# Kernel optimization log

Hardware: AMD Instinct MI355X
Metric: run time of the kernel (lower is better)

## Reference

```python
import jax, jax.numpy as jnp
import numpy as np

N_CELLS = 500_000
B = 512
D_X = 128
D_Z = 32
D_IN = D_X + D_Z  # 160
H = 256
D_OUT = 16


def _linear_params(key, fan_in, fan_out):
    k1, k2 = jax.random.split(key)
    bound = 1.0 / np.sqrt(fan_in)
    W = jax.random.uniform(k1, (fan_in, fan_out), jnp.float32, -bound, bound)
    b = jax.random.uniform(k2, (fan_out,), jnp.float32, -bound, bound)
    return W, b


def setup_inputs() -> dict:
    key = jax.random.key(0)
    ks = jax.random.split(key, 8)
    X = jax.random.uniform(ks[0], (N_CELLS, D_X), jnp.float32)  # nonneg counts-like
    Z = jax.random.normal(ks[1], (B, D_Z), jnp.float32)
    cell_to_batch = jax.random.randint(ks[2], (N_CELLS,), 0, B, jnp.int64)
    sample_idx_batch = jnp.arange(B, dtype=jnp.int64)
    W1, b1 = _linear_params(ks[3], D_IN, H)
    W2, b2 = _linear_params(ks[4], H, H)
    W3, b3 = _linear_params(ks[5], H, D_OUT)
    return {"X": X, "Z": Z, "W1": W1, "b1": b1, "W2": W2, "b2": b2,
            "W3": W3, "b3": b3, "cell_to_batch": cell_to_batch,
            "sample_idx_batch": sample_idx_batch}


def reference(X, Z, W1, b1, W2, b2, W3, b3, cell_to_batch, sample_idx_batch):
    # gather per-sample covariates to per-cell rows
    Zc = Z[cell_to_batch]                              # [N, D_Z]
    seg = sample_idx_batch[cell_to_batch]              # [N] remapped sample ids
    # preprocessor: log-normalize X, concat covariates
    Xp = jnp.concatenate([jnp.log1p(X), Zc], axis=-1)  # [N, D_IN]
    # cell predictor MLP (Linear-ReLU x2 + Linear)
    h = jax.nn.relu(Xp @ W1 + b1)
    h = jax.nn.relu(h @ W2 + b2)
    X_cell = h @ W3 + b3                               # [N, D_OUT]
    # aggregator: segment mean over cells of each sample
    nseg = sample_idx_batch.shape[0]
    sums = jax.ops.segment_sum(X_cell, seg, num_segments=nseg)
    counts = jax.ops.segment_sum(jnp.ones((X_cell.shape[0], 1), X_cell.dtype), seg, num_segments=nseg)
    Y_sample = sums / jnp.maximum(counts, 1.0)
    # postprocessor: identity
    return Y_sample
```

## Files before the change

### kernel.cpp

```cpp
#include <hip/hip_runtime.h>
#include <hip/hip_bf16.h>

typedef __attribute__((ext_vector_type(8))) short short8;
typedef __attribute__((ext_vector_type(4))) short short4v;
typedef __attribute__((ext_vector_type(4))) float floatx4;

#define N_CELLS  500000
#define B_SAMP   512
#define D_X      128
#define D_Z      32
#define H_DIM    256
#define D_OUT    16

#define M_TILE   64
#define NBLK     7813
#define LDA      136
#define LDH      264
#define SP_LD    20

#define NREP     64

#define OFF_W1P   0
#define OFF_W2P   65536
#define OFF_W3P   196608
#define OFF_ZW    204800
#define OFF_ACC   729088
#define OFF_CNT   2826240
#define OFF_C2S   2957312

#define W1_BLKS   128
#define W2_BLKS   256
#define W3_BLKS   16
#define ZW_BLKS   512
#define C2S_BLKS  1954

__device__ __forceinline__ short bfb(float x) {
    union { __hip_bfloat16 h; short s; } u;
    u.h = __float2bfloat16(x);
    return u.s;
}

__global__ __launch_bounds__(256)
void prep(const float* __restrict__ W1, const float* __restrict__ b1,
          const float* __restrict__ W2, const float* __restrict__ W3,
          const float* __restrict__ Z,
          const int* __restrict__ c2b, const int* __restrict__ sidx,
          __hip_bfloat16* __restrict__ w1p, __hip_bfloat16* __restrict__ w2p,
          __hip_bfloat16* __restrict__ w3p, float* __restrict__ zw1,
          float* __restrict__ cnts, int* __restrict__ c2s) {
    int bid = blockIdx.x;
    int tid = threadIdx.x;
    if (bid < W1_BLKS + W2_BLKS + W3_BLKS) {
        const float* W; __hip_bfloat16* dst; int N, kS, idx; float scale;
        if (bid < W1_BLKS) {
            idx = bid * 256 + tid; W = W1; dst = w1p; N = H_DIM; kS = 4;
            scale = 0.6931471805599453f;
        } else if (bid < W1_BLKS + W2_BLKS) {
            idx = (bid - W1_BLKS) * 256 + tid; W = W2; dst = w2p; N = H_DIM; kS = 8;
            scale = 1.0f;
        } else {
            idx = (bid - W1_BLKS - W2_BLKS) * 256 + tid; W = W3; dst = w3p; N = D_OUT; kS = 8;
            scale = 1.0f;
        }
        int j = idx & 7;
        int L = (idx >> 3) & 63;
        int s = (idx >> 9) % kS;
        int t = idx / (kS << 9);
        int k = s * 32 + ((L >> 4) << 3) + j;
        int n = t * 16 + (L & 15);
        dst[idx] = __float2bfloat16(W[(size_t)k * N + n] * scale);
        return;
    }
    bid -= W1_BLKS + W2_BLKS + W3_BLKS;
    if (bid < ZW_BLKS) {
        int s = bid;
        float a = b1[tid];
        const float* zr = Z + (size_t)s * D_Z;
        const float* wr = W1 + (size_t)D_X * H_DIM + tid;
#pragma unroll 8
        for (int k = 0; k < D_Z; ++k) a += zr[k] * wr[(size_t)k * H_DIM];
        zw1[(size_t)s * H_DIM + tid] = a;
        return;
    }
    bid -= ZW_BLKS;
    int i = bid * 256 + tid;
    if (i < N_CELLS) {
        int si = sidx[c2b[i]];
        c2s[i] = si;
        atomicAdd(&cnts[(size_t)(bid & (NREP - 1)) * B_SAMP + si], 1.0f);
    }
}

__global__ __launch_bounds__(512, 6)
void fused_mlp(const float* __restrict__ X, const int* __restrict__ c2b,
               const int* __restrict__ c2s, const float* __restrict__ b2,
               const float* __restrict__ b3,
               const __hip_bfloat16* __restrict__ w1p,
               const __hip_bfloat16* __restrict__ w2p,
               const __hip_bfloat16* __restrict__ w3p,
               const float* __restrict__ zw1,
               float* __restrict__ accs, float* __restrict__ cnts) {
    __shared__ __align__(16) short sX[M_TILE * LDA];
    __shared__ short sH[M_TILE][LDH];
    __shared__ int sSI[M_TILE];
    short (*xp)[LDA] = (short (*)[LDA])sX;
    float (*sP)[M_TILE][SP_LD] = (float (*)[M_TILE][SP_LD])sX;

    const int tid = threadIdx.x;
    const int w   = tid >> 6;
    const int L   = tid & 63;
    const int q   = L >> 4;
    const int ln  = L & 15;
    const int wm  = w >> 2;
    const int wn  = w & 3;
    const int base = blockIdx.x * M_TILE;

    int g0 = base + wm * 32 + ln;      if (g0 >= N_CELLS) g0 = N_CELLS - 1;
    int g1 = base + wm * 32 + 16 + ln; if (g1 >= N_CELLS) g1 = N_CELLS - 1;
    int cb0 = c2b[g0];
    int cb1 = c2b[g1];
    floatx4 acc[2][4];
#pragma unroll
    for (int nt = 0; nt < 4; ++nt) {
        acc[0][nt] = *(const floatx4*)(zw1 + (size_t)cb0 * H_DIM + wn * 64 + nt * 16 + q * 4);
        acc[1][nt] = *(const floatx4*)(zw1 + (size_t)cb1 * H_DIM + wn * 64 + nt * 16 + q * 4);
    }

#pragma unroll
    for (int i = 0; i < 4; ++i) {
        int idx = tid + i * 512;
        int row = idx >> 5, c4 = idx & 31;
        int gr = base + row; if (gr >= N_CELLS) gr = N_CELLS - 1;
        float4 v = *(const float4*)(X + (size_t)gr * D_X + c4 * 4);
        short4v pk;
        pk.x = bfb(__log2f(1.0f + v.x));
        pk.y = bfb(__log2f(1.0f + v.y));
        pk.z = bfb(__log2f(1.0f + v.z));
        pk.w = bfb(__log2f(1.0f + v.w));
        *(short4v*)&xp[row][c4 * 4] = pk;
    }
    if ((tid & 7) == 0) {
        int row = tid >> 3;
        int gr = base + row; if (gr >= N_CELLS) gr = N_CELLS - 1;
        sSI[row] = c2s[gr];
    }
    __syncthreads();

#pragma unroll
    for (int s = 0; s < 4; ++s) {
        short8 x0 = *(const short8*)&xp[wm * 32 + ln][s * 32 + q * 8];
        short8 x1 = *(const short8*)&xp[wm * 32 + 16 + ln][s * 32 + q * 8];
#pragma unroll
        for (int nt = 0; nt < 4; ++nt) {
            short8 wf = *(const short8*)(w1p + (size_t)(((((wn * 4 + nt) * 4) + s) << 6) + L) * 8);
            acc[0][nt] = __builtin_amdgcn_mfma_f32_16x16x32_bf16(wf, x0, acc[0][nt], 0, 0, 0);
            acc[1][nt] = __builtin_amdgcn_mfma_f32_16x16x32_bf16(wf, x1, acc[1][nt], 0, 0, 0);
        }
    }
#pragma unroll
    for (int nt = 0; nt < 4; ++nt) {
        short4v p0, p1;
        p0.x = bfb(fmaxf(acc[0][nt][0], 0.f));
        p0.y = bfb(fmaxf(acc[0][nt][1], 0.f));
        p0.z = bfb(fmaxf(acc[0][nt][2], 0.f));
        p0.w = bfb(fmaxf(acc[0][nt][3], 0.f));
        p1.x = bfb(fmaxf(acc[1][nt][0], 0.f));
        p1.y = bfb(fmaxf(acc[1][nt][1], 0.f));
        p1.z = bfb(fmaxf(acc[1][nt][2], 0.f));
        p1.w = bfb(fmaxf(acc[1][nt][3], 0.f));
        *(short4v*)&sH[wm * 32 + ln][wn * 64 + nt * 16 + q * 4] = p0;
        *(short4v*)&sH[wm * 32 + 16 + ln][wn * 64 + nt * 16 + q * 4] = p1;
    }
    __syncthreads();

#pragma unroll
    for (int nt = 0; nt < 4; ++nt) {
        float4 bv = *(const float4*)(b2 + wn * 64 + nt * 16 + q * 4);
        acc[0][nt] = (floatx4){bv.x, bv.y, bv.z, bv.w};
        acc[1][nt] = acc[0][nt];
    }
#pragma unroll
    for (int s = 0; s < 8; ++s) {
        short8 x0 = *(const short8*)&sH[wm * 32 + ln][s * 32 + q * 8];
        short8 x1 = *(const short8*)&sH[wm * 32 + 16 + ln][s * 32 + q * 8];
#pragma unroll
        for (int nt = 0; nt < 4; ++nt) {
            short8 wf = *(const short8*)(w2p + (size_t)(((((wn * 4 + nt) * 8) + s) << 6) + L) * 8);
            acc[0][nt] = __builtin_amdgcn_mfma_f32_16x16x32_bf16(wf, x0, acc[0][nt], 0, 0, 0);
            acc[1][nt] = __builtin_amdgcn_mfma_f32_16x16x32_bf16(wf, x1, acc[1][nt], 0, 0, 0);
        }
    }
    __syncthreads();
#pragma unroll
    for (int nt = 0; nt < 4; ++nt) {
        short4v p0, p1;
        p0.x = bfb(fmaxf(acc[0][nt][0], 0.f));
        p0.y = bfb(fmaxf(acc[0][nt][1], 0.f));
        p0.z = bfb(fmaxf(acc[0][nt][2], 0.f));
        p0.w = bfb(fmaxf(acc[0][nt][3], 0.f));
        p1.x = bfb(fmaxf(acc[1][nt][0], 0.f));
        p1.y = bfb(fmaxf(acc[1][nt][1], 0.f));
        p1.z = bfb(fmaxf(acc[1][nt][2], 0.f));
        p1.w = bfb(fmaxf(acc[1][nt][3], 0.f));
        *(short4v*)&sH[wm * 32 + ln][wn * 64 + nt * 16 + q * 4] = p0;
        *(short4v*)&sH[wm * 32 + 16 + ln][wn * 64 + nt * 16 + q * 4] = p1;
    }
    __syncthreads();

    {
        int g  = w & 3;
        int kh = w >> 2;
        floatx4 a3 = (floatx4){0.f, 0.f, 0.f, 0.f};
#pragma unroll
        for (int ss = 0; ss < 4; ++ss) {
            int s = kh * 4 + ss;
            short8 hv = *(const short8*)&sH[g * 16 + ln][s * 32 + q * 8];
            short8 wf = *(const short8*)(w3p + (size_t)((s << 6) + L) * 8);
            a3 = __builtin_amdgcn_mfma_f32_16x16x32_bf16(wf, hv, a3, 0, 0, 0);
        }
#pragma unroll
        for (int r = 0; r < 4; ++r)
            sP[kh][g * 16 + ln][q * 4 + r] = a3[r];
    }
    __syncthreads();

    {
        int rep = blockIdx.x & (NREP - 1);
        float* accR = accs + (size_t)rep * (B_SAMP * D_OUT);
#pragma unroll
        for (int i = 0; i < 2; ++i) {
            int idx = tid + i * 512;
            int m = idx >> 4, n = idx & 15;
            int cell = base + m;
            if (cell < N_CELLS) {
                float v = sP[0][m][n] + sP[1][m][n] + b3[n];
                atomicAdd(&accR[(size_t)sSI[m] * D_OUT + n], v);
            }
        }
    }
}

__global__ __launch_bounds__(256)
void finalize(const float* __restrict__ accs, const float* __restrict__ cnts,
              float* __restrict__ out) {
    int o = blockIdx.x * blockDim.x + threadIdx.x;
    int s = o >> 4;
    float sum = 0.f, cnt = 0.f;
#pragma unroll 8
    for (int r = 0; r < NREP; ++r) {
        sum += accs[(size_t)r * (B_SAMP * D_OUT) + o];
        cnt += cnts[(size_t)r * B_SAMP + s];
    }
    out[o] = sum / fmaxf(cnt, 1.0f);
}

extern "C" void kernel_launch(void* const* d_in, const int* in_sizes, int n_in,
                              void* d_out, int out_size, void* d_ws, size_t ws_size,
                              hipStream_t stream) {
    const float* X   = (const float*)d_in[0];
    const float* Z   = (const float*)d_in[1];
    const float* W1  = (const float*)d_in[2];
    const float* b1  = (const float*)d_in[3];
    const float* W2  = (const float*)d_in[4];
    const float* b2  = (const float*)d_in[5];
    const float* W3  = (const float*)d_in[6];
    const float* b3  = (const float*)d_in[7];
    const int*   c2b = (const int*)d_in[8];
    const int*   sidx= (const int*)d_in[9];

    char* ws = (char*)d_ws;
    __hip_bfloat16* w1p = (__hip_bfloat16*)(ws + OFF_W1P);
    __hip_bfloat16* w2p = (__hip_bfloat16*)(ws + OFF_W2P);
    __hip_bfloat16* w3p = (__hip_bfloat16*)(ws + OFF_W3P);
    float* zw1  = (float*)(ws + OFF_ZW);
    float* accs = (float*)(ws + OFF_ACC);
    float* cnts = (float*)(ws + OFF_CNT);
    int*   c2s  = (int*)(ws + OFF_C2S);
    float* out  = (float*)d_out;

    hipMemsetAsync(accs, 0, (size_t)NREP * (B_SAMP * D_OUT + B_SAMP) * 4, stream);

    prep<<<W1_BLKS + W2_BLKS + W3_BLKS + ZW_BLKS + C2S_BLKS, 256, 0, stream>>>(
        W1, b1, W2, W3, Z, c2b, sidx, w1p, w2p, w3p, zw1, cnts, c2s);

    fused_mlp<<<NBLK, 512, 0, stream>>>(X, c2b, c2s, b2, b3,
                                        w1p, w2p, w3p, zw1, accs, cnts);
    finalize<<<32, 256, 0, stream>>>(accs, cnts, out);
}
```

Measured before the change: 525.7 us.

## Double cell tile to 128 rows, alias X into sH, shuffle-feed layer 3

Result: no change. 532.1 us (+1.2%).

```diff
diff --git a/kernel.cpp b/kernel.cpp
--- a/kernel.cpp
+++ b/kernel.cpp
@@ -12,9 +12,8 @@
 #define H_DIM    256
 #define D_OUT    16
 
-#define M_TILE   64
-#define NBLK     7813
-#define LDA      136
+#define M_TILE   128
+#define NBLK     3907
 #define LDH      264
 #define SP_LD    20
 
@@ -38,6 +37,9 @@
     union { __hip_bfloat16 h; short s; } u;
     u.h = __float2bfloat16(x);
     return u.s;
+}
+__device__ __forceinline__ int pack2(float a, float b) {
+    return ((int)(unsigned short)bfb(a)) | ((int)bfb(b) << 16);
 }
 
 __global__ __launch_bounds__(256)
@@ -91,7 +93,7 @@
     }
 }
 
-__global__ __launch_bounds__(512, 6)
+__global__ __launch_bounds__(512, 4)
 void fused_mlp(const float* __restrict__ X, const int* __restrict__ c2b,
                const int* __restrict__ c2s, const float* __restrict__ b2,
                const float* __restrict__ b3,
@@ -100,11 +102,9 @@
                const __hip_bfloat16* __restrict__ w3p,
                const float* __restrict__ zw1,
                float* __restrict__ accs, float* __restrict__ cnts) {
-    __shared__ __align__(16) short sX[M_TILE * LDA];
-    __shared__ short sH[M_TILE][LDH];
+    __shared__ __align__(16) short sH[M_TILE][LDH];
     __shared__ int sSI[M_TILE];
-    short (*xp)[LDA] = (short (*)[LDA])sX;
-    float (*sP)[M_TILE][SP_LD] = (float (*)[M_TILE][SP_LD])sX;
+    float (*sP)[M_TILE][SP_LD] = (float (*)[M_TILE][SP_LD])sH;
 
     const int tid = threadIdx.x;
     const int w   = tid >> 6;
@@ -115,19 +115,19 @@
     const int wn  = w & 3;
     const int base = blockIdx.x * M_TILE;
 
-    int g0 = base + wm * 32 + ln;      if (g0 >= N_CELLS) g0 = N_CELLS - 1;
-    int g1 = base + wm * 32 + 16 + ln; if (g1 >= N_CELLS) g1 = N_CELLS - 1;
-    int cb0 = c2b[g0];
-    int cb1 = c2b[g1];
-    floatx4 acc[2][4];
-#pragma unroll
-    for (int nt = 0; nt < 4; ++nt) {
-        acc[0][nt] = *(const floatx4*)(zw1 + (size_t)cb0 * H_DIM + wn * 64 + nt * 16 + q * 4);
-        acc[1][nt] = *(const floatx4*)(zw1 + (size_t)cb1 * H_DIM + wn * 64 + nt * 16 + q * 4);
-    }
-
-#pragma unroll
-    for (int i = 0; i < 4; ++i) {
+    floatx4 acc[4][4];
+#pragma unroll
+    for (int mt = 0; mt < 4; ++mt) {
+        int g = base + wm * 64 + mt * 16 + ln;
+        if (g >= N_CELLS) g = N_CELLS - 1;
+        int cbm = c2b[g];
+#pragma unroll
+        for (int nt = 0; nt < 4; ++nt)
+            acc[mt][nt] = *(const floatx4*)(zw1 + (size_t)cbm * H_DIM + wn * 64 + nt * 16 + q * 4);
+    }
+
+#pragma unroll
+    for (int i = 0; i < 8; ++i) {
         int idx = tid + i * 512;
         int row = idx >> 5, c4 = idx & 31;
         int gr = base + row; if (gr >= N_CELLS) gr = N_CELLS - 1;
@@ -137,40 +137,40 @@
         pk.y = bfb(__log2f(1.0f + v.y));
         pk.z = bfb(__log2f(1.0f + v.z));
         pk.w = bfb(__log2f(1.0f + v.w));
-        *(short4v*)&xp[row][c4 * 4] = pk;
-    }
-    if ((tid & 7) == 0) {
-        int row = tid >> 3;
-        int gr = base + row; if (gr >= N_CELLS) gr = N_CELLS - 1;
-        sSI[row] = c2s[gr];
+        *(short4v*)&sH[row][c4 * 4] = pk;
+    }
+    if (tid < M_TILE) {
+        int gr = base + tid; if (gr >= N_CELLS) gr = N_CELLS - 1;
+        sSI[tid] = c2s[gr];
     }
     __syncthreads();
 
 #pragma unroll
     for (int s = 0; s < 4; ++s) {
-        short8 x0 = *(const short8*)&xp[wm * 32 + ln][s * 32 + q * 8];
-        short8 x1 = *(const short8*)&xp[wm * 32 + 16 + ln][s * 32 + q * 8];
+        short8 xv[4];
+#pragma unroll
+        for (int mt = 0; mt < 4; ++mt)
+            xv[mt] = *(const short8*)&sH[wm * 64 + mt * 16 + ln][s * 32 + q * 8];
 #pragma unroll
         for (int nt = 0; nt < 4; ++nt) {
             short8 wf = *(const short8*)(w1p + (size_t)(((((wn * 4 + nt) * 4) + s) << 6) + L) * 8);
-            acc[0][nt] = __builtin_amdgcn_mfma_f32_16x16x32_bf16(wf, x0, acc[0][nt], 0, 0, 0);
-            acc[1][nt] = __builtin_amdgcn_mfma_f32_16x16x32_bf16(wf, x1, acc[1][nt], 0, 0, 0);
-        }
-    }
-#pragma unroll
-    for (int nt = 0; nt < 4; ++nt) {
-        short4v p0, p1;
-        p0.x = bfb(fmaxf(acc[0][nt][0], 0.f));
-        p0.y = bfb(fmaxf(acc[0][nt][1], 0.f));
-        p0.z = bfb(fmaxf(acc[0][nt][2], 0.f));
-        p0.w = bfb(fmaxf(acc[0][nt][3], 0.f));
-        p1.x = bfb(fmaxf(acc[1][nt][0], 0.f));
-        p1.y = bfb(fmaxf(acc[1][nt][1], 0.f));
-        p1.z = bfb(fmaxf(acc[1][nt][2], 0.f));
-        p1.w = bfb(fmaxf(acc[1][nt][3], 0.f));
-        *(short4v*)&sH[wm * 32 + ln][wn * 64 + nt * 16 + q * 4] = p0;
-        *(short4v*)&sH[wm * 32 + 16 + ln][wn * 64 + nt * 16 + q * 4] = p1;
-    }
+#pragma unroll
+            for (int mt = 0; mt < 4; ++mt)
+                acc[mt][nt] = __builtin_amdgcn_mfma_f32_16x16x32_bf16(wf, xv[mt], acc[mt][nt], 0, 0, 0);
+        }
+    }
+    __syncthreads();
+#pragma unroll
+    for (int mt = 0; mt < 4; ++mt)
+#pragma unroll
+        for (int nt = 0; nt < 4; ++nt) {
+            short4v pk;
+            pk.x = bfb(fmaxf(acc[mt][nt][0], 0.f));
+            pk.y = bfb(fmaxf(acc[mt][nt][1], 0.f));
+            pk.z = bfb(fmaxf(acc[mt][nt][2], 0.f));
+            pk.w = bfb(fmaxf(acc[mt][nt][3], 0.f));
+            *(short4v*)&sH[wm * 64 + mt * 16 + ln][wn * 64 + nt * 16 + q * 4] = pk;
+        }
     __syncthreads();
 
 #pragma unroll
@@ -178,62 +178,75 @@
         float4 bv = *(const float4*)(b2 + wn * 64 + nt * 16 + q * 4);
         acc[0][nt] = (floatx4){bv.x, bv.y, bv.z, bv.w};
         acc[1][nt] = acc[0][nt];
+        acc[2][nt] = acc[0][nt];
+        acc[3][nt] = acc[0][nt];
     }
 #pragma unroll
     for (int s = 0; s < 8; ++s) {
-        short8 x0 = *(const short8*)&sH[wm * 32 + ln][s * 32 + q * 8];
-        short8 x1 = *(const short8*)&sH[wm * 32 + 16 + ln][s * 32 + q * 8];
+        short8 xv[4];
+#pragma unroll
+        for (int mt = 0; mt < 4; ++mt)
+            xv[mt] = *(const short8*)&sH[wm * 64 + mt * 16 + ln][s * 32 + q * 8];
 #pragma unroll
         for (int nt = 0; nt < 4; ++nt) {
             short8 wf = *(const short8*)(w2p + (size_t)(((((wn * 4 + nt) * 8) + s) << 6) + L) * 8);
-            acc[0][nt] = __builtin_amdgcn_mfma_f32_16x16x32_bf16(wf, x0, acc[0][nt], 0, 0, 0);
-            acc[1][nt] = __builtin_amdgcn_mfma_f32_16x16x32_bf16(wf, x1, acc[1][nt], 0, 0, 0);
-        }
-    }
-    __syncthreads();
-#pragma unroll
-    for (int nt = 0; nt < 4; ++nt) {
-        short4v p0, p1;
-        p0.x = bfb(fmaxf(acc[0][nt][0], 0.f));
-        p0.y = bfb(fmaxf(acc[0][nt][1], 0.f));
-        p0.z = bfb(fmaxf(acc[0][nt][2], 0.f));
-        p0.w = bfb(fmaxf(acc[0][nt][3], 0.f));
-        p1.x = bfb(fmaxf(acc[1][nt][0], 0.f));
-        p1.y = bfb(fmaxf(acc[1][nt][1], 0.f));
-        p1.z = bfb(fmaxf(acc[1][nt][2], 0.f));
-        p1.w = bfb(fmaxf(acc[1][nt][3], 0.f));
-        *(short4v*)&sH[wm * 32 + ln][wn * 64 + nt * 16 + q * 4] = p0;
-        *(short4v*)&sH[wm * 32 + 16 + ln][wn * 64 + nt * 16 + q * 4] = p1;
-    }
-    __syncthreads();
-
-    {
-        int g  = w & 3;
-        int kh = w >> 2;
-        floatx4 a3 = (floatx4){0.f, 0.f, 0.f, 0.f};
-#pragma unroll
-        for (int ss = 0; ss < 4; ++ss) {
-            int s = kh * 4 + ss;
-            short8 hv = *(const short8*)&sH[g * 16 + ln][s * 32 + q * 8];
-            short8 wf = *(const short8*)(w3p + (size_t)((s << 6) + L) * 8);
-            a3 = __builtin_amdgcn_mfma_f32_16x16x32_bf16(wf, hv, a3, 0, 0, 0);
-        }
-#pragma unroll
-        for (int r = 0; r < 4; ++r)
-            sP[kh][g * 16 + ln][q * 4 + r] = a3[r];
-    }
+#pragma unroll
+            for (int mt = 0; mt < 4; ++mt)
+                acc[mt][nt] = __builtin_amdgcn_mfma_f32_16x16x32_bf16(wf, xv[mt], acc[mt][nt], 0, 0, 0);
+        }
+    }
+
+    int pk[4][4][2];
+#pragma unroll
+    for (int mt = 0; mt < 4; ++mt)
+#pragma unroll
+        for (int nt = 0; nt < 4; ++nt) {
+            pk[mt][nt][0] = pack2(fmaxf(acc[mt][nt][0], 0.f), fmaxf(acc[mt][nt][1], 0.f));
+            pk[mt][nt][1] = pack2(fmaxf(acc[mt][nt][2], 0.f), fmaxf(acc[mt][nt][3], 0.f));
+        }
+    const int lane0 = (((2 * q) & 3) << 4) + ln;
+    const int lane1 = (((2 * q + 1) & 3) << 4) + ln;
+    const bool hi = (q >> 1) != 0;
+    floatx4 p3[4];
+#pragma unroll
+    for (int mt = 0; mt < 4; ++mt) p3[mt] = (floatx4){0.f, 0.f, 0.f, 0.f};
+#pragma unroll
+    for (int h = 0; h < 2; ++h) {
+        short8 wf = *(const short8*)(w3p + (size_t)(((2 * wn + h) << 6) + L) * 8);
+#pragma unroll
+        for (int mt = 0; mt < 4; ++mt) {
+            int a0 = __shfl(pk[mt][2 * h][0], lane0);
+            int c0 = __shfl(pk[mt][2 * h + 1][0], lane0);
+            int a1 = __shfl(pk[mt][2 * h][1], lane0);
+            int c1 = __shfl(pk[mt][2 * h + 1][1], lane0);
+            int a2 = __shfl(pk[mt][2 * h][0], lane1);
+            int c2 = __shfl(pk[mt][2 * h + 1][0], lane1);
+            int a3 = __shfl(pk[mt][2 * h][1], lane1);
+            int c3 = __shfl(pk[mt][2 * h + 1][1], lane1);
+            union { int i[4]; short8 s; } u;
+            u.i[0] = hi ? c0 : a0;
+            u.i[1] = hi ? c1 : a1;
+            u.i[2] = hi ? c2 : a2;
+            u.i[3] = hi ? c3 : a3;
+            p3[mt] = __builtin_amdgcn_mfma_f32_16x16x32_bf16(wf, u.s, p3[mt], 0, 0, 0);
+        }
+    }
+    __syncthreads();
+#pragma unroll
+    for (int mt = 0; mt < 4; ++mt)
+        *(floatx4*)&sP[wn][wm * 64 + mt * 16 + ln][q * 4] = p3[mt];
     __syncthreads();
 
     {
         int rep = blockIdx.x & (NREP - 1);
         float* accR = accs + (size_t)rep * (B_SAMP * D_OUT);
 #pragma unroll
-        for (int i = 0; i < 2; ++i) {
+        for (int i = 0; i < 4; ++i) {
             int idx = tid + i * 512;
             int m = idx >> 4, n = idx & 15;
             int cell = base + m;
             if (cell < N_CELLS) {
-                float v = sP[0][m][n] + sP[1][m][n] + b3[n];
+                float v = sP[0][m][n] + sP[1][m][n] + sP[2][m][n] + sP[3][m][n] + b3[n];
                 atomicAdd(&accR[(size_t)sSI[m] * D_OUT + n], v);
             }
         }
```

## Software-pipeline weight fragment loads across MFMA k-steps and layers

Applied to the files above, without the earlier changes.

Measured after the change: 508.8 us. 1.03x faster.

```diff
diff --git a/kernel.cpp b/kernel.cpp
--- a/kernel.cpp
+++ b/kernel.cpp
@@ -91,7 +91,7 @@
     }
 }
 
-__global__ __launch_bounds__(512, 6)
+__global__ __launch_bounds__(512, 4)
 void fused_mlp(const float* __restrict__ X, const int* __restrict__ c2b,
                const int* __restrict__ c2s, const float* __restrict__ b2,
                const float* __restrict__ b3,
@@ -115,6 +115,11 @@
     const int wn  = w & 3;
     const int base = blockIdx.x * M_TILE;
 
+    short8 wfc[4], wfn[4];
+#pragma unroll
+    for (int nt = 0; nt < 4; ++nt)
+        wfc[nt] = *(const short8*)(w1p + (size_t)((((wn * 4 + nt) * 4) << 6) + L) * 8);
+
     int g0 = base + wm * 32 + ln;      if (g0 >= N_CELLS) g0 = N_CELLS - 1;
     int g1 = base + wm * 32 + 16 + ln; if (g1 >= N_CELLS) g1 = N_CELLS - 1;
     int cb0 = c2b[g0];
@@ -125,6 +130,7 @@
         acc[0][nt] = *(const floatx4*)(zw1 + (size_t)cb0 * H_DIM + wn * 64 + nt * 16 + q * 4);
         acc[1][nt] = *(const floatx4*)(zw1 + (size_t)cb1 * H_DIM + wn * 64 + nt * 16 + q * 4);
     }
+    float b3v = b3[tid & 15];
 
 #pragma unroll
     for (int i = 0; i < 4; ++i) {
@@ -139,24 +145,38 @@
         pk.w = bfb(__log2f(1.0f + v.w));
         *(short4v*)&xp[row][c4 * 4] = pk;
     }
-    if ((tid & 7) == 0) {
-        int row = tid >> 3;
-        int gr = base + row; if (gr >= N_CELLS) gr = N_CELLS - 1;
-        sSI[row] = c2s[gr];
+    if (tid < M_TILE) {
+        int gr = base + tid; if (gr >= N_CELLS) gr = N_CELLS - 1;
+        sSI[tid] = c2s[gr];
     }
     __syncthreads();
 
 #pragma unroll
     for (int s = 0; s < 4; ++s) {
+        if (s < 3) {
+#pragma unroll
+            for (int nt = 0; nt < 4; ++nt)
+                wfn[nt] = *(const short8*)(w1p + (size_t)(((((wn * 4 + nt) * 4) + s + 1) << 6) + L) * 8);
+        }
         short8 x0 = *(const short8*)&xp[wm * 32 + ln][s * 32 + q * 8];
         short8 x1 = *(const short8*)&xp[wm * 32 + 16 + ln][s * 32 + q * 8];
 #pragma unroll
         for (int nt = 0; nt < 4; ++nt) {
-            short8 wf = *(const short8*)(w1p + (size_t)(((((wn * 4 + nt) * 4) + s) << 6) + L) * 8);
-            acc[0][nt] = __builtin_amdgcn_mfma_f32_16x16x32_bf16(wf, x0, acc[0][nt], 0, 0, 0);
-            acc[1][nt] = __builtin_amdgcn_mfma_f32_16x16x32_bf16(wf, x1, acc[1][nt], 0, 0, 0);
-        }
-    }
+            acc[0][nt] = __builtin_amdgcn_mfma_f32_16x16x32_bf16(wfc[nt], x0, acc[0][nt], 0, 0, 0);
+            acc[1][nt] = __builtin_amdgcn_mfma_f32_16x16x32_bf16(wfc[nt], x1, acc[1][nt], 0, 0, 0);
+        }
+        if (s < 3) {
+#pragma unroll
+            for (int nt = 0; nt < 4; ++nt) wfc[nt] = wfn[nt];
+        }
+    }
+#pragma unroll
+    for (int nt = 0; nt < 4; ++nt)
+        wfc[nt] = *(const short8*)(w2p + (size_t)((((wn * 4 + nt) * 8) << 6) + L) * 8);
+    float4 bv[4];
+#pragma unroll
+    for (int nt = 0; nt < 4; ++nt)
+        bv[nt] = *(const float4*)(b2 + wn * 64 + nt * 16 + q * 4);
 #pragma unroll
     for (int nt = 0; nt < 4; ++nt) {
         short4v p0, p1;
@@ -173,22 +193,32 @@
     }
     __syncthreads();
 
+    const int kh = w >> 2;
 #pragma unroll
     for (int nt = 0; nt < 4; ++nt) {
-        float4 bv = *(const float4*)(b2 + wn * 64 + nt * 16 + q * 4);
-        acc[0][nt] = (floatx4){bv.x, bv.y, bv.z, bv.w};
+        acc[0][nt] = (floatx4){bv[nt].x, bv[nt].y, bv[nt].z, bv[nt].w};
         acc[1][nt] = acc[0][nt];
     }
 #pragma unroll
     for (int s = 0; s < 8; ++s) {
+        if (s < 7) {
+#pragma unroll
+            for (int nt = 0; nt < 4; ++nt)
+                wfn[nt] = *(const short8*)(w2p + (size_t)(((((wn * 4 + nt) * 8) + s + 1) << 6) + L) * 8);
+        } else {
+#pragma unroll
+            for (int ss = 0; ss < 4; ++ss)
+                wfn[ss] = *(const short8*)(w3p + (size_t)(((kh * 4 + ss) << 6) + L) * 8);
+        }
         short8 x0 = *(const short8*)&sH[wm * 32 + ln][s * 32 + q * 8];
         short8 x1 = *(const short8*)&sH[wm * 32 + 16 + ln][s * 32 + q * 8];
 #pragma unroll
         for (int nt = 0; nt < 4; ++nt) {
-            short8 wf = *(const short8*)(w2p + (size_t)(((((wn * 4 + nt) * 8) + s) << 6) + L) * 8);
-            acc[0][nt] = __builtin_amdgcn_mfma_f32_16x16x32_bf16(wf, x0, acc[0][nt], 0, 0, 0);
-            acc[1][nt] = __builtin_amdgcn_mfma_f32_16x16x32_bf16(wf, x1, acc[1][nt], 0, 0, 0);
-        }
+            acc[0][nt] = __builtin_amdgcn_mfma_f32_16x16x32_bf16(wfc[nt], x0, acc[0][nt], 0, 0, 0);
+            acc[1][nt] = __builtin_amdgcn_mfma_f32_16x16x32_bf16(wfc[nt], x1, acc[1][nt], 0, 0, 0);
+        }
+#pragma unroll
+        for (int nt = 0; nt < 4; ++nt) wfc[nt] = wfn[nt];
     }
     __syncthreads();
 #pragma unroll
@@ -208,19 +238,15 @@
     __syncthreads();
 
     {
-        int g  = w & 3;
-        int kh = w >> 2;
+        int g = w & 3;
         floatx4 a3 = (floatx4){0.f, 0.f, 0.f, 0.f};
 #pragma unroll
         for (int ss = 0; ss < 4; ++ss) {
             int s = kh * 4 + ss;
             short8 hv = *(const short8*)&sH[g * 16 + ln][s * 32 + q * 8];
-            short8 wf = *(const short8*)(w3p + (size_t)((s << 6) + L) * 8);
-            a3 = __builtin_amdgcn_mfma_f32_16x16x32_bf16(wf, hv, a3, 0, 0, 0);
-        }
-#pragma unroll
-        for (int r = 0; r < 4; ++r)
-            sP[kh][g * 16 + ln][q * 4 + r] = a3[r];
+            a3 = __builtin_amdgcn_mfma_f32_16x16x32_bf16(wfc[ss], hv, a3, 0, 0, 0);
+        }
+        *(floatx4*)&sP[kh][g * 16 + ln][q * 4] = a3;
     }
     __syncthreads();
 
@@ -233,7 +259,7 @@
             int m = idx >> 4, n = idx & 15;
             int cell = base + m;
             if (cell < N_CELLS) {
-                float v = sP[0][m][n] + sP[1][m][n] + b3[n];
+                float v = sP[0][m][n] + sP[1][m][n] + b3v;
                 atomicAdd(&accR[(size_t)sSI[m] * D_OUT + n], v);
             }
         }
```
